# Kernel tuning notes

Measured on AMD Instinct MI355X. Metric: run time of the kernel, lower is better.

Reference implementation:

```python
import jax, jax.numpy as jnp
import numpy as np

STRIDE = 2

def setup_inputs() -> dict:
    key = jax.random.key(0)
    k1, k2 = jax.random.split(key)
    x = jax.random.normal(k1, (32, 128, 112, 112), dtype=jnp.float32)
    # matches nn.init.normal_(std=0.1)
    weight = jax.random.normal(k2, (256, 128, 3, 3), dtype=jnp.float32) * 0.1
    return {"x": x, "weight": weight}

def reference(x, weight):
    # Equivalent to the tile-loop: valid cross-correlation, no bias, stride=STRIDE.
    # x: (B, Cin, H, W); weight: (Cout, Cin, k, k) -> (B, Cout, w, w)
    return jax.lax.conv_general_dilated(
        x, weight,
        window_strides=(STRIDE, STRIDE),
        padding="VALID",
        dimension_numbers=("NCHW", "OIHW", "NCHW"),
    )
```

## Files before the change

### kernel.cpp

```cpp
#include <hip/hip_runtime.h>


#define BATCH 32
#define CIN   128
#define H     112
#define W     112
#define COUT  256
#define OH    55
#define OW    55
#define NPIX  (OH*OW)
#define NTOT  (BATCH*NPIX)

#define BM    128
#define BN    192
#define NB_N  ((NTOT + BN - 1) / BN)
#define NBLK  (2 * NB_N)

typedef __bf16 bf16x8 __attribute__((ext_vector_type(8)));
typedef float  f32x4  __attribute__((ext_vector_type(4)));

__device__ __forceinline__ unsigned short f2bf(float f) {
    unsigned u = __float_as_uint(f);
    u += 0x7FFFu + ((u >> 16) & 1u);
    return (unsigned short)(u >> 16);
}

__device__ __forceinline__ void gld_lds16(const void* g, void* l) {
    __builtin_amdgcn_global_load_lds((__attribute__((address_space(1))) void*)g,
                                     (__attribute__((address_space(3))) void*)l,
                                     16, 0, 0);
}

#define XP 136
#define WBLK ((9*COUT*CIN + 255)/256)
__global__ __launch_bounds__(256) void relayout_k(const float* __restrict__ x,
                                                  const float* __restrict__ w,
                                                  unsigned short* __restrict__ xs,
                                                  unsigned short* __restrict__ wt) {
    if (blockIdx.x >= BATCH * H) {
        int o = (blockIdx.x - BATCH * H) * 256 + threadIdx.x;
        if (o < 9 * COUT * CIN) {
            int cin  = o & (CIN - 1);
            int r    = o >> 7;
            int cout = r & (COUT - 1);
            int tap  = r >> 8;
            wt[o] = f2bf(w[((size_t)cout * CIN + cin) * 9 + tap]);
        }
        return;
    }
    __shared__ __align__(16) unsigned short tile[W * XP];
    const int bh = blockIdx.x;
    const int b  = bh / H;
    const int h  = bh - b * H;
    const float* xr = x + (size_t)b * CIN * (H * W) + (size_t)h * W;
    const int t = threadIdx.x;
#pragma unroll
    for (int i = 0; i < 7; ++i) {
        int e  = t + i * 256;
        int cp = e / 28;
        int w4 = e - cp * 28;
        int c  = cp * 2;
        float4 v0 = *(const float4*)(xr + (size_t)c * (H * W) + w4 * 4);
        float4 v1 = *(const float4*)(xr + (size_t)(c + 1) * (H * W) + w4 * 4);
        int c8 = c >> 3;
        int cl = c & 7;
        float a0[4] = {v0.x, v0.y, v0.z, v0.w};
        float a1[4] = {v1.x, v1.y, v1.z, v1.w};
#pragma unroll
        for (int j = 0; j < 4; ++j) {
            int ww  = w4 * 4 + j;
            int idx = ww * XP + ((c8 + 2 * ww) & 15) * 8 + cl;
            *(ushort2*)(tile + idx) = (ushort2){f2bf(a0[j]), f2bf(a1[j])};
        }
    }
    __syncthreads();
    uint4* dst = (uint4*)(xs + (size_t)bh * (W * CIN));
#pragma unroll
    for (int i = 0; i < 7; ++i) {
        int e  = t + i * 256;
        int ww = e >> 4;
        int c8 = e & 15;
        dst[e] = *(const uint4*)(tile + ww * XP + ((c8 + 2 * ww) & 15) * 8);
    }
}

__global__ __launch_bounds__(256, 2) void conv_mfma_k(const unsigned short* __restrict__ xs,
                                                      const unsigned short* __restrict__ wt,
                                                      float* __restrict__ out) {
    __shared__ __align__(16) unsigned short L[2][(BM + BN) * 64];

    const int tid  = threadIdx.x;
    const int wave = tid >> 6;
    const int lane = tid & 63;
    const int wm   = wave >> 1;
    const int wn   = wave & 1;
    const int lrow = lane & 15;
    const int kg   = lane >> 4;

    const int xcd = blockIdx.x & 7;
    const int lin = blockIdx.x >> 3;
    const int q = NBLK >> 3, r = NBLK & 7;
    const int bswz = (xcd < r ? xcd * (q + 1) : r * (q + 1) + (xcd - r) * q) + lin;
    const int m0 = (bswz & 1) * BM;
    const int n0 = (bswz >> 1) * BN;

    const int rA  = tid >> 3;
    const int sx8 = ((tid & 7) ^ (rA & 7)) * 8;
    int xbr[6];
#pragma unroll
    for (int c = 0; c < 6; ++c) {
        int nn = n0 + c * 32 + rA;
        if (nn >= NTOT) nn = NTOT - 1;
        int b  = nn / NPIX;
        int rp = nn - b * NPIX;
        int oh = rp / OW;
        int ow = rp - oh * OW;
        xbr[c] = ((b * H + 2 * oh) * W + 2 * ow) * CIN;
    }

    auto stage = [&](int kt, int buf) {
        const int tap  = kt >> 1;
        const int cin0 = (kt & 1) * 64;
        const int r2   = (tap >= 6) ? 2 : (tap >= 3) ? 1 : 0;
        const int s    = tap - 3 * r2;
        const unsigned short* wsrc = wt + tap * (COUT * CIN) + (m0 + rA) * CIN + cin0 + sx8;
        const unsigned short* xsrc = xs + (r2 * W + s) * CIN + cin0 + sx8;
        unsigned short* lb = &L[buf][0];
#pragma unroll
        for (int c = 0; c < 4; ++c)
            gld_lds16(wsrc + c * 32 * CIN, lb + c * 2048 + wave * 512);
#pragma unroll
        for (int c = 0; c < 6; ++c)
            gld_lds16(xsrc + xbr[c], lb + BM * 64 + c * 2048 + wave * 512);
    };

    const int aoff = (wm * 64 + lrow) * 64;
    const int boff = BM * 64 + (wn * 96 + lrow) * 64;
    const int sxk0 = ((0 * 4 + kg) ^ (lrow & 7)) * 8;
    const int sxk1 = ((1 * 4 + kg) ^ (lrow & 7)) * 8;

    f32x4 acc[4][6];
#pragma unroll
    for (int mi = 0; mi < 4; ++mi)
#pragma unroll
        for (int ni = 0; ni < 6; ++ni)
            acc[mi][ni] = (f32x4){0.f, 0.f, 0.f, 0.f};

    stage(0, 0);
    stage(1, 1);

#pragma unroll 2
    for (int kt = 0; kt < 18; ++kt) {
        const int buf = kt & 1;
        if (kt == 17) asm volatile("s_waitcnt vmcnt(0)" ::: "memory");
        else          asm volatile("s_waitcnt vmcnt(10)" ::: "memory");
        asm volatile("s_barrier" ::: "memory");

        const unsigned short* Lb = &L[buf][0];
        bf16x8 a0[4], a1[4], b0[6], b1[6];
#pragma unroll
        for (int mi = 0; mi < 4; ++mi) {
            a0[mi] = *(const bf16x8*)(Lb + aoff + mi * 1024 + sxk0);
            a1[mi] = *(const bf16x8*)(Lb + aoff + mi * 1024 + sxk1);
        }
#pragma unroll
        for (int ni = 0; ni < 6; ++ni) {
            b0[ni] = *(const bf16x8*)(Lb + boff + ni * 1024 + sxk0);
            b1[ni] = *(const bf16x8*)(Lb + boff + ni * 1024 + sxk1);
        }
        asm volatile("s_barrier" ::: "memory");
        if (kt + 2 < 18) stage(kt + 2, buf);
        __builtin_amdgcn_s_setprio(1);
#pragma unroll
        for (int mi = 0; mi < 4; ++mi)
#pragma unroll
            for (int ni = 0; ni < 6; ++ni)
                acc[mi][ni] = __builtin_amdgcn_mfma_f32_16x16x32_bf16(a0[mi], b0[ni], acc[mi][ni], 0, 0, 0);
#pragma unroll
        for (int mi = 0; mi < 4; ++mi)
#pragma unroll
            for (int ni = 0; ni < 6; ++ni)
                acc[mi][ni] = __builtin_amdgcn_mfma_f32_16x16x32_bf16(a1[mi], b1[ni], acc[mi][ni], 0, 0, 0);
        __builtin_amdgcn_s_setprio(0);
    }

    long obase[6];
    int  okn[6];
#pragma unroll
    for (int ni = 0; ni < 6; ++ni) {
        int nn = n0 + wn * 96 + ni * 16 + lrow;
        okn[ni] = (nn < NTOT);
        if (!okn[ni]) nn = 0;
        int b   = nn / NPIX;
        int pix = nn - b * NPIX;
        obase[ni] = (long)b * (COUT * NPIX) + pix;
    }
    const int mrow = kg * 4;
#pragma unroll
    for (int mi = 0; mi < 4; ++mi) {
#pragma unroll
        for (int rr = 0; rr < 4; ++rr) {
            int  m  = m0 + wm * 64 + mi * 16 + mrow + rr;
            long mo = (long)m * NPIX;
#pragma unroll
            for (int ni = 0; ni < 6; ++ni)
                if (okn[ni]) out[obase[ni] + mo] = acc[mi][ni][rr];
        }
    }
}

__global__ __launch_bounds__(256) void direct_k(const float* __restrict__ x,
                                                const float* __restrict__ w,
                                                float* __restrict__ out) {
    const int pix = blockIdx.x * 256 + threadIdx.x;
    if (pix >= NPIX) return;
    const int b = blockIdx.z, cout0 = blockIdx.y * 8;
    const int oh = pix / OW, ow = pix - oh * OW;
    float acc[8];
#pragma unroll
    for (int i = 0; i < 8; ++i) acc[i] = 0.f;
    const float* xbp = x + ((size_t)b * CIN) * (H * W) + (size_t)(oh * 2) * W + ow * 2;
    const float* wb  = w + (size_t)cout0 * (CIN * 9);
    for (int cin = 0; cin < CIN; ++cin) {
        const float* xp = xbp + (size_t)cin * (H * W);
        float xv[9];
#pragma unroll
        for (int r = 0; r < 3; ++r) {
            xv[r * 3 + 0] = xp[r * W + 0];
            xv[r * 3 + 1] = xp[r * W + 1];
            xv[r * 3 + 2] = xp[r * W + 2];
        }
#pragma unroll
        for (int c = 0; c < 8; ++c) {
            const float* wp = wb + (size_t)c * (CIN * 9) + cin * 9;
#pragma unroll
            for (int k = 0; k < 9; ++k) acc[c] = fmaf(wp[k], xv[k], acc[c]);
        }
    }
    const size_t ob = ((size_t)b * COUT + cout0) * NPIX + pix;
#pragma unroll
    for (int c = 0; c < 8; ++c) out[ob + (size_t)c * NPIX] = acc[c];
}

extern "C" void kernel_launch(void* const* d_in, const int* in_sizes, int n_in,
                              void* d_out, int out_size, void* d_ws, size_t ws_size,
                              hipStream_t stream) {
    const float* x = (const float*)d_in[0];
    const float* w = (const float*)d_in[1];
    float* out = (float*)d_out;

    const size_t xs_elems = (size_t)BATCH * H * W * CIN;
    const size_t wt_elems = (size_t)9 * COUT * CIN;
    const size_t need = (xs_elems + wt_elems) * 2;

    if (ws_size >= need) {
        unsigned short* xs = (unsigned short*)d_ws;
        unsigned short* wt = xs + xs_elems;
        relayout_k<<<dim3(BATCH * H + WBLK), dim3(256), 0, stream>>>(x, w, xs, wt);
        conv_mfma_k<<<dim3(NBLK), dim3(256), 0, stream>>>(xs, wt, out);
    } else {
        dim3 grid((NPIX + 255) / 256, COUT / 8, BATCH);
        direct_k<<<grid, dim3(256), 0, stream>>>(x, w, out);
    }
}
```

Baseline: 383.8 us.

## Load activation fragments directly to registers using channel-plane parity-split layout

The activation transform now writes a channel-group-major layout with each row split into even and odd columns, so that stride-2 output pixels become contiguous 16-byte chunks. The GEMM kernel then loads the B operand straight from global memory into registers, double-buffered across k-steps, and keeps only the weight tile in LDS. This cuts LDS capacity and LDS read traffic and may allow more blocks per CU. In exchange it relies on the cache for the B reuse shared by the two M-blocks and across waves, and it raises register pressure from the 24 bf16x8 B buffers per thread.

```diff
diff --git a/kernel.cpp b/kernel.cpp
--- a/kernel.cpp
+++ b/kernel.cpp
@@ -15,6 +15,9 @@
 #define BN    192
 #define NB_N  ((NTOT + BN - 1) / BN)
 #define NBLK  (2 * NB_N)
+
+#define CPLANE (BATCH*H*112)
+#define BSTRIDE (H*112)
 
 typedef __bf16 bf16x8 __attribute__((ext_vector_type(8)));
 typedef float  f32x4  __attribute__((ext_vector_type(4)));
@@ -74,20 +77,21 @@
         }
     }
     __syncthreads();
-    uint4* dst = (uint4*)(xs + (size_t)bh * (W * CIN));
+    uint4* xsq = (uint4*)xs;
 #pragma unroll
     for (int i = 0; i < 7; ++i) {
         int e  = t + i * 256;
-        int ww = e >> 4;
-        int c8 = e & 15;
-        dst[e] = *(const uint4*)(tile + ww * XP + ((c8 + 2 * ww) & 15) * 8);
+        int c8 = e / 112;
+        int ww = e - c8 * 112;
+        int idx = c8 * CPLANE + (b * H + h) * 112 + (ww & 1) * 56 + (ww >> 1);
+        xsq[idx] = *(const uint4*)(tile + ww * XP + ((c8 + 2 * ww) & 15) * 8);
     }
 }
 
 __global__ __launch_bounds__(256, 2) void conv_mfma_k(const unsigned short* __restrict__ xs,
                                                       const unsigned short* __restrict__ wt,
                                                       float* __restrict__ out) {
-    __shared__ __align__(16) unsigned short L[2][(BM + BN) * 64];
+    __shared__ __align__(16) unsigned short L[2][BM * 64];
 
     const int tid  = threadIdx.x;
     const int wave = tid >> 6;
@@ -106,38 +110,43 @@
 
     const int rA  = tid >> 3;
     const int sx8 = ((tid & 7) ^ (rA & 7)) * 8;
-    int xbr[6];
-#pragma unroll
-    for (int c = 0; c < 6; ++c) {
-        int nn = n0 + c * 32 + rA;
+    auto stageA = [&](int kt, int buf) {
+        const int tap  = kt >> 1;
+        const int cin0 = (kt & 1) * 64;
+        const unsigned short* wsrc = wt + tap * (COUT * CIN) + (m0 + rA) * CIN + cin0 + sx8;
+        unsigned short* lb = &L[buf][0];
+#pragma unroll
+        for (int c = 0; c < 4; ++c)
+            gld_lds16(wsrc + c * 32 * CIN, lb + c * 2048 + wave * 512);
+    };
+
+    int C0[6];
+#pragma unroll
+    for (int ni = 0; ni < 6; ++ni) {
+        int nn = n0 + wn * 96 + ni * 16 + lrow;
         if (nn >= NTOT) nn = NTOT - 1;
         int b  = nn / NPIX;
         int rp = nn - b * NPIX;
         int oh = rp / OW;
         int ow = rp - oh * OW;
-        xbr[c] = ((b * H + 2 * oh) * W + 2 * ow) * CIN;
-    }
-
-    auto stage = [&](int kt, int buf) {
-        const int tap  = kt >> 1;
-        const int cin0 = (kt & 1) * 64;
-        const int r2   = (tap >= 6) ? 2 : (tap >= 3) ? 1 : 0;
-        const int s    = tap - 3 * r2;
-        const unsigned short* wsrc = wt + tap * (COUT * CIN) + (m0 + rA) * CIN + cin0 + sx8;
-        const unsigned short* xsrc = xs + (r2 * W + s) * CIN + cin0 + sx8;
-        unsigned short* lb = &L[buf][0];
-#pragma unroll
-        for (int c = 0; c < 4; ++c)
-            gld_lds16(wsrc + c * 32 * CIN, lb + c * 2048 + wave * 512);
-#pragma unroll
-        for (int c = 0; c < 6; ++c)
-            gld_lds16(xsrc + xbr[c], lb + BM * 64 + c * 2048 + wave * 512);
+        C0[ni] = b * BSTRIDE + oh * 224 + ow + kg * CPLANE;
+    }
+
+    auto issueB = [&](int kt, bf16x8* Br) {
+        const int tap = kt >> 1;
+        const int r2  = (tap >= 6) ? 2 : (tap >= 3) ? 1 : 0;
+        const int s   = tap - 3 * r2;
+        const int sc  = r2 * 112 + (s & 1) * 56 + (s >> 1) + (kt & 1) * (8 * CPLANE);
+#pragma unroll
+        for (int kh = 0; kh < 2; ++kh)
+#pragma unroll
+            for (int ni = 0; ni < 6; ++ni)
+                Br[kh * 6 + ni] = *(const bf16x8*)(xs + (size_t)(C0[ni] + sc + kh * (4 * CPLANE)) * 8);
     };
 
     const int aoff = (wm * 64 + lrow) * 64;
-    const int boff = BM * 64 + (wn * 96 + lrow) * 64;
-    const int sxk0 = ((0 * 4 + kg) ^ (lrow & 7)) * 8;
-    const int sxk1 = ((1 * 4 + kg) ^ (lrow & 7)) * 8;
+    const int sxk0 = ((0 + kg) ^ (lrow & 7)) * 8;
+    const int sxk1 = ((4 + kg) ^ (lrow & 7)) * 8;
 
     f32x4 acc[4][6];
 #pragma unroll
@@ -146,42 +155,68 @@
         for (int ni = 0; ni < 6; ++ni)
             acc[mi][ni] = (f32x4){0.f, 0.f, 0.f, 0.f};
 
-    stage(0, 0);
-    stage(1, 1);
-
-#pragma unroll 2
-    for (int kt = 0; kt < 18; ++kt) {
-        const int buf = kt & 1;
-        if (kt == 17) asm volatile("s_waitcnt vmcnt(0)" ::: "memory");
-        else          asm volatile("s_waitcnt vmcnt(10)" ::: "memory");
+    bf16x8 Bc[12], Bn[12];
+    stageA(0, 0);
+    issueB(0, Bc);
+    stageA(1, 1);
+
+    for (int kt2 = 0; kt2 < 18; kt2 += 2) {
+        issueB(kt2 + 1, Bn);
+        asm volatile("s_waitcnt vmcnt(16)" ::: "memory");
         asm volatile("s_barrier" ::: "memory");
-
-        const unsigned short* Lb = &L[buf][0];
-        bf16x8 a0[4], a1[4], b0[6], b1[6];
-#pragma unroll
-        for (int mi = 0; mi < 4; ++mi) {
-            a0[mi] = *(const bf16x8*)(Lb + aoff + mi * 1024 + sxk0);
-            a1[mi] = *(const bf16x8*)(Lb + aoff + mi * 1024 + sxk1);
-        }
-#pragma unroll
-        for (int ni = 0; ni < 6; ++ni) {
-            b0[ni] = *(const bf16x8*)(Lb + boff + ni * 1024 + sxk0);
-            b1[ni] = *(const bf16x8*)(Lb + boff + ni * 1024 + sxk1);
+        {
+            const unsigned short* Lb = &L[0][0];
+            bf16x8 a0[4], a1[4];
+#pragma unroll
+            for (int mi = 0; mi < 4; ++mi) {
+                a0[mi] = *(const bf16x8*)(Lb + aoff + mi * 1024 + sxk0);
+                a1[mi] = *(const bf16x8*)(Lb + aoff + mi * 1024 + sxk1);
+            }
+            asm volatile("s_barrier" ::: "memory");
+            if (kt2 + 2 < 18) stageA(kt2 + 2, 0);
+            __builtin_amdgcn_s_setprio(1);
+#pragma unroll
+            for (int mi = 0; mi < 4; ++mi)
+#pragma unroll
+                for (int ni = 0; ni < 6; ++ni)
+                    acc[mi][ni] = __builtin_amdgcn_mfma_f32_16x16x32_bf16(a0[mi], Bc[ni], acc[mi][ni], 0, 0, 0);
+#pragma unroll
+            for (int mi = 0; mi < 4; ++mi)
+#pragma unroll
+                for (int ni = 0; ni < 6; ++ni)
+                    acc[mi][ni] = __builtin_amdgcn_mfma_f32_16x16x32_bf16(a1[mi], Bc[6 + ni], acc[mi][ni], 0, 0, 0);
+            __builtin_amdgcn_s_setprio(0);
+        }
+        if (kt2 + 2 < 18) {
+            issueB(kt2 + 2, Bc);
+            asm volatile("s_waitcnt vmcnt(16)" ::: "memory");
+        } else {
+            asm volatile("s_waitcnt vmcnt(0)" ::: "memory");
         }
         asm volatile("s_barrier" ::: "memory");
-        if (kt + 2 < 18) stage(kt + 2, buf);
-        __builtin_amdgcn_s_setprio(1);
-#pragma unroll
-        for (int mi = 0; mi < 4; ++mi)
-#pragma unroll
-            for (int ni = 0; ni < 6; ++ni)
-                acc[mi][ni] = __builtin_amdgcn_mfma_f32_16x16x32_bf16(a0[mi], b0[ni], acc[mi][ni], 0, 0, 0);
-#pragma unroll
-        for (int mi = 0; mi < 4; ++mi)
-#pragma unroll
-            for (int ni = 0; ni < 6; ++ni)
-                acc[mi][ni] = __builtin_amdgcn_mfma_f32_16x16x32_bf16(a1[mi], b1[ni], acc[mi][ni], 0, 0, 0);
-        __builtin_amdgcn_s_setprio(0);
+        {
+            const unsigned short* Lb = &L[1][0];
+            bf16x8 a0[4], a1[4];
+#pragma unroll
+            for (int mi = 0; mi < 4; ++mi) {
+                a0[mi] = *(const bf16x8*)(Lb + aoff + mi * 1024 + sxk0);
+                a1[mi] = *(const bf16x8*)(Lb + aoff + mi * 1024 + sxk1);
+            }
+            asm volatile("s_barrier" ::: "memory");
+            if (kt2 + 3 < 18) stageA(kt2 + 3, 1);
+            __builtin_amdgcn_s_setprio(1);
+#pragma unroll
+            for (int mi = 0; mi < 4; ++mi)
+#pragma unroll
+                for (int ni = 0; ni < 6; ++ni)
+                    acc[mi][ni] = __builtin_amdgcn_mfma_f32_16x16x32_bf16(a0[mi], Bn[ni], acc[mi][ni], 0, 0, 0);
+#pragma unroll
+            for (int mi = 0; mi < 4; ++mi)
+#pragma unroll
+                for (int ni = 0; ni < 6; ++ni)
+                    acc[mi][ni] = __builtin_amdgcn_mfma_f32_16x16x32_bf16(a1[mi], Bn[6 + ni], acc[mi][ni], 0, 0, 0);
+            __builtin_amdgcn_s_setprio(0);
+        }
     }
 
     long obase[6];
```

New measurement: 460.6 us. 1.2x slower.
